# Performance work log

Hardware: AMD Instinct MI355X
Metric: run time of the kernel (lower is better)

Reference implementation:

```python
import jax, jax.numpy as jnp
import numpy as np

B = 512       # batch_size
IN = 256      # input_size
H = 512       # hidden_size
OUT = 64      # output_size
N_PAIRS = B - 1   # number of H0 persistence deaths (connected components merges)
TOL = 1e-6    # rtol for torch.isclose
ATOL = 1e-8   # torch default atol
EPS = 0.0     # homology_eps
TARGET_P = 1.0
HOM_P = 1.0
COMP_P = 0.01

_IU = np.triu_indices(B, 1)  # condensed pdist indexing, static


def _mlp(batch, W1, b1, W2, b2, W3, b3, Wout, bout):
    # FeedForward: input->hidden, (n_layers-1) hidden->hidden, hidden->output, ReLU
    h = jax.nn.relu(batch @ W1 + b1)
    h = jax.nn.relu(h @ W2 + b2)
    h = jax.nn.relu(h @ W3 + b3)
    return h @ Wout + bout


def _pdist(y):
    # condensed euclidean pairwise distances, same ordering as torch F.pdist
    d = y[_IU[0]] - y[_IU[1]]                 # [P, OUT]
    return jnp.sqrt(jnp.sum(d * d, axis=-1))  # [P]


def setup_inputs() -> dict:
    key = jax.random.key(0)
    ks = jax.random.split(key, 8)
    batch = jax.random.normal(ks[0], (B, IN), jnp.float32)
    target = jax.random.normal(ks[1], (B, OUT), jnp.float32)
    W1 = jax.random.normal(ks[2], (IN, H), jnp.float32) / np.sqrt(IN)
    W2 = jax.random.normal(ks[3], (H, H), jnp.float32) / np.sqrt(H)
    W3 = jax.random.normal(ks[4], (H, H), jnp.float32) / np.sqrt(H)
    Wout = jax.random.normal(ks[5], (H, OUT), jnp.float32) / np.sqrt(H)
    b1 = jnp.zeros((H,), jnp.float32)
    b2 = jnp.zeros((H,), jnp.float32)
    b3 = jnp.zeros((H,), jnp.float32)
    bout = jnp.zeros((OUT,), jnp.float32)
    # persistence deaths = actual critical pdist values (from the external
    # Vietoris-Rips routine in the original); sample N_PAIRS distinct entries.
    y0 = _mlp(batch, W1, b1, W2, b2, W3, b3, Wout, bout)
    pd0 = np.asarray(_pdist(y0))
    idx = np.random.default_rng(0).choice(pd0.shape[0], N_PAIRS, replace=False)
    persistence_deaths = jnp.asarray(pd0[idx], jnp.float32)
    return {"batch": batch, "target": target,
            "W1": W1, "b1": b1, "W2": W2, "b2": b2, "W3": W3, "b3": b3,
            "Wout": Wout, "bout": bout,
            "persistence_deaths": persistence_deaths}


def reference(batch, target, W1, b1, W2, b2, W3, b3, Wout, bout, persistence_deaths):
    y = _mlp(batch, W1, b1, W2, b2, W3, b3, Wout, bout)   # [B, OUT]
    y_hom = y  # normalize_for_homology = False
    pd = _pdist(y_hom)                                     # [P]
    # vectorized indicator_death over all pairs (replaces per-pair Python loop)
    mask = jnp.any(jnp.isclose(pd[:, None], persistence_deaths[None, :],
                               rtol=TOL, atol=ATOL), axis=1)      # [P] bool
    # homology_dim=0: birth_pdist = 0; norm=1 of selected (death - 0 + eps)
    homology_loss = jnp.sum(jnp.abs(jnp.where(mask, pd + EPS, 0.0)))
    target_loss = jnp.mean((target - y) ** 2)
    compactness_loss = jnp.sum(jnp.abs(y - jnp.mean(y, axis=0, keepdims=True)))
    loss = TARGET_P * target_loss + HOM_P * homology_loss + COMP_P * compactness_loss
    return loss
```

## Files before the change

kernel.cpp:

```cpp
#include <hip/hip_runtime.h>

#define B_    512
#define IN_   256
#define H_    512
#define OUT_  64
#define NDEATH (B_ - 1)
#define NSORT  512
#define RTOL_ 1e-6
#define ATOL_ 1e-8
#define NBLK  256
#define KT    32

typedef __attribute__((ext_vector_type(4))) double d4_t;

__device__ __forceinline__ void ast(double* p, double v) {
    __hip_atomic_store(p, v, __ATOMIC_RELAXED, __HIP_MEMORY_SCOPE_AGENT);
}

__device__ __forceinline__ void gbar(unsigned* cnt, unsigned nb) {
    __syncthreads();
    if (threadIdx.x == 0) {
        __hip_atomic_fetch_add(cnt, 1u, __ATOMIC_RELAXED,
                               __HIP_MEMORY_SCOPE_AGENT);
        while (__hip_atomic_load(cnt, __ATOMIC_RELAXED,
                                 __HIP_MEMORY_SCOPE_AGENT) < nb)
            __builtin_amdgcn_s_sleep(2);
    }
    __syncthreads();
}

__device__ void sort_windows(const float* __restrict__ deaths,
                             double* sd, double* slo, double* shi, int t) {
    int i1 = t + 256;
    sd[t]  = (t  < NDEATH) ? (double)deaths[t]  : 1e300;
    sd[i1] = (i1 < NDEATH) ? (double)deaths[i1] : 1e300;
    __syncthreads();
    for (int k = 2; k <= NSORT; k <<= 1) {
        for (int j = k >> 1; j > 0; j >>= 1) {
            int l = ((t & ~(j - 1)) << 1) | (t & (j - 1));
            int p = l + j;
            bool up = ((l & k) == 0);
            double a = sd[l], b = sd[p];
            if ((a > b) == up) { sd[l] = b; sd[p] = a; }
            __syncthreads();
        }
    }
    for (int i = t; i < NSORT; i += 256) {
        double d = sd[i];
        double w = ATOL_ + RTOL_ * fabs(d);
        slo[i] = d - w;
        shi[i] = d + w;
    }
    __syncthreads();
}

template <typename TIN, bool RELU>
__device__ void gemm_dev(const TIN* __restrict__ A, const float* __restrict__ W,
                         const float* __restrict__ bias, double* __restrict__ C,
                         int N, int K, int tile, int t,
                         double (&As)[2][KT][33], double (&Ws)[2][KT][33]) {
    const int lane = t & 63;
    const int wave = t >> 6;
    const int wm   = wave & 1, wn = wave >> 1;
    const int nbx  = N >> 5;
    const int row0 = (tile / nbx) << 5;
    const int col0 = (tile % nbx) << 5;

    const int akk = t & 31;
    const int amm = t >> 5;
    const int wnn = t & 31;
    const int wkk = t >> 5;
    const int nkt = K >> 5;

    TIN   ar[2][4];
    float wr[2][4];

    auto load_to = [&](int rs, int kt) {
        const int k0 = kt << 5;
        #pragma unroll
        for (int p = 0; p < 4; ++p) {
            ar[rs][p] = A[(size_t)(row0 + amm + 8 * p) * K + k0 + akk];
            wr[rs][p] = W[(size_t)(k0 + wkk + 8 * p) * N + col0 + wnn];
        }
    };
    auto stage = [&](int rs, int buf) {
        #pragma unroll
        for (int p = 0; p < 4; ++p) {
            As[buf][akk][amm + 8 * p] = (double)ar[rs][p];
            Ws[buf][wkk + 8 * p][wnn] = (double)wr[rs][p];
        }
    };

    load_to(0, 0);
    if (nkt > 1) load_to(1, 1);
    stage(0, 0);
    __syncthreads();

    d4_t c4 = {0.0, 0.0, 0.0, 0.0};
    const int mrow = wm * 16 + (lane & 15);
    const int ncol = wn * 16 + (lane & 15);
    const int kq   = lane >> 4;

    for (int kt = 0; kt < nkt; ++kt) {
        const int cur = kt & 1;
        if (kt + 2 < nkt) load_to(cur, kt + 2);
        #pragma unroll
        for (int ks = 0; ks < KT / 4; ++ks) {
            double av = As[cur][ks * 4 + kq][mrow];
            double bv = Ws[cur][ks * 4 + kq][ncol];
            c4 = __builtin_amdgcn_mfma_f64_16x16x4f64(av, bv, c4, 0, 0, 0);
        }
        __syncthreads();
        if (kt + 1 < nkt) stage(cur ^ 1, cur ^ 1);
        __syncthreads();
    }

    #pragma unroll
    for (int r = 0; r < 4; ++r) {
        int row = row0 + wm * 16 + (lane >> 4) * 4 + r;
        int col = col0 + wn * 16 + (lane & 15);
        double v = c4[r] + (double)bias[col];
        if (RELU) v = v > 0.0 ? v : 0.0;
        ast(&C[(size_t)row * N + col], v);
    }
}

__device__ void mc_dev(const float* __restrict__ target,
                       const double* __restrict__ y,
                       double* __restrict__ t_part, double* __restrict__ c_part,
                       int c, int t) {
    const int wave = t >> 6, lane = t & 63;
    double v0 = y[(size_t)t * OUT_ + c];
    double v1 = y[(size_t)(t + 256) * OUT_ + c];
    double s = v0 + v1;
    for (int off = 32; off; off >>= 1) s += __shfl_down(s, off);
    __shared__ double swm[4];
    __shared__ double smean;
    if (lane == 0) swm[wave] = s;
    __syncthreads();
    if (t == 0) smean = (swm[0] + swm[1] + swm[2] + swm[3]) / (double)B_;
    __syncthreads();
    double m = smean;
    double d0 = (double)target[(size_t)t * OUT_ + c] - v0;
    double d1 = (double)target[(size_t)(t + 256) * OUT_ + c] - v1;
    double t_s = d0 * d0 + d1 * d1;
    double c_s = fabs(v0 - m) + fabs(v1 - m);
    for (int off = 32; off; off >>= 1) {
        t_s += __shfl_down(t_s, off);
        c_s += __shfl_down(c_s, off);
    }
    __shared__ double st[4], sc[4];
    if (lane == 0) { st[wave] = t_s; sc[wave] = c_s; }
    __syncthreads();
    if (t == 0) {
        ast(&t_part[c], st[0] + st[1] + st[2] + st[3]);
        ast(&c_part[c], sc[0] + sc[1] + sc[2] + sc[3]);
    }
}

__device__ __forceinline__ double pair_val(const double* __restrict__ yrow_s,
                                           const double* __restrict__ yj,
                                           const double* __restrict__ slo,
                                           const double* __restrict__ shi) {
    double s = 0.0;
    #pragma unroll
    for (int d = 0; d < OUT_; d += 2) {
        double2 v = *(const double2*)(yj + d);
        double d0 = yrow_s[d]     - v.x;
        double d1 = yrow_s[d + 1] - v.y;
        s = fma(d0, d0, s);
        s = fma(d1, d1, s);
    }
    double pd = sqrt(s);
    int pos = 0;
    #pragma unroll
    for (int step = NSORT / 2; step; step >>= 1) {
        if (slo[pos + step - 1] <= pd) pos += step;
    }
    bool m = (pos > 0) && (shi[pos - 1] >= pd);
    return m ? pd : 0.0;
}

__device__ void pdist_dev(const double* __restrict__ y,
                          double* __restrict__ hom_part, int bid, int t,
                          double* yA, double* yB,
                          const double* slo, const double* shi) {
    const int iA = bid;
    const int iB = 510 - bid;
    if (t < OUT_)            yA[t]        = y[(size_t)iA * OUT_ + t];
    else if (t < 2 * OUT_)   yB[t - OUT_] = y[(size_t)iB * OUT_ + (t - OUT_)];
    __syncthreads();

    double local = 0.0;
    for (int j = iA + 1 + t; j < B_; j += 256)
        local += pair_val(yA, y + (size_t)j * OUT_, slo, shi);
    if (iB != iA)
        for (int j = iB + 1 + t; j < B_; j += 256)
            local += pair_val(yB, y + (size_t)j * OUT_, slo, shi);

    for (int off = 32; off; off >>= 1) local += __shfl_down(local, off);
    __shared__ double sw[4];
    int wave = t >> 6, lane = t & 63;
    if (lane == 0) sw[wave] = local;
    __syncthreads();
    if (t == 0) ast(&hom_part[bid], sw[0] + sw[1] + sw[2] + sw[3]);
}

__global__ __launch_bounds__(256) void fused_k(
    const float* __restrict__ batch, const float* __restrict__ target,
    const float* __restrict__ W1, const float* __restrict__ b1,
    const float* __restrict__ W2, const float* __restrict__ b2,
    const float* __restrict__ W3, const float* __restrict__ b3,
    const float* __restrict__ Wout, const float* __restrict__ bout,
    const float* __restrict__ deaths, float* __restrict__ out,
    double* __restrict__ hA, double* __restrict__ hB,
    double* __restrict__ hC, double* __restrict__ yv,
    double* __restrict__ hom_part, double* __restrict__ t_part,
    double* __restrict__ c_part, unsigned* __restrict__ cnt) {
    const int bid = blockIdx.x;
    const int t   = threadIdx.x;
    const int g   = bid >> 4;
    const int c   = bid & 15;
    unsigned* gc  = cnt + g * 32;

    __shared__ double As[2][KT][33];
    __shared__ double Ws[2][KT][33];
    __shared__ double slo[NSORT], shi[NSORT];
    __shared__ double yA[OUT_], yB[OUT_];
    __shared__ int    lastf;
    double* sd = &As[0][0][0];

    gemm_dev<float,  true>(batch, W1, b1, hA, H_, IN_, bid, t, As, Ws);
    gbar(&gc[0], 16);
    gemm_dev<double, true>(hA, W2, b2, hB, H_, H_, bid, t, As, Ws);
    gbar(&gc[1], 16);
    gemm_dev<double, true>(hB, W3, b3, hC, H_, H_, bid, t, As, Ws);
    gbar(&gc[2], 16);

    if (c < 2) gemm_dev<double, false>(hC, Wout, bout, yv, OUT_, H_, g * 2 + c, t, As, Ws);
    else       sort_windows(deaths, sd, slo, shi, t);

    gbar(&cnt[512], NBLK);
    if (c < 2) sort_windows(deaths, sd, slo, shi, t);

    pdist_dev(yv, hom_part, bid, t, yA, yB, slo, shi);
    if (bid < OUT_) mc_dev(target, yv, t_part, c_part, bid, t);

    __syncthreads();
    if (t == 0) {
        unsigned prev = __hip_atomic_fetch_add(&cnt[544], 1u, __ATOMIC_RELAXED,
                                               __HIP_MEMORY_SCOPE_AGENT);
        lastf = (prev == NBLK - 1);
    }
    __syncthreads();
    if (lastf) {
        double h  = __hip_atomic_load(&hom_part[t], __ATOMIC_RELAXED,
                                      __HIP_MEMORY_SCOPE_AGENT);
        double tp = 0.0, cp = 0.0;
        if (t < OUT_) {
            tp = __hip_atomic_load(&t_part[t], __ATOMIC_RELAXED,
                                   __HIP_MEMORY_SCOPE_AGENT);
            cp = __hip_atomic_load(&c_part[t], __ATOMIC_RELAXED,
                                   __HIP_MEMORY_SCOPE_AGENT);
        }
        for (int off = 32; off; off >>= 1) {
            h  += __shfl_down(h,  off);
            tp += __shfl_down(tp, off);
            cp += __shfl_down(cp, off);
        }
        __shared__ double sh[4], stp[4], scp[4];
        int wave = t >> 6, lane = t & 63;
        if (lane == 0) { sh[wave] = h; stp[wave] = tp; scp[wave] = cp; }
        __syncthreads();
        if (t == 0) {
            double hs = sh[0]  + sh[1]  + sh[2]  + sh[3];
            double ts = stp[0] + stp[1] + stp[2] + stp[3];
            double cs = scp[0] + scp[1] + scp[2] + scp[3];
            out[0] = (float)(ts / (double)(B_ * OUT_) + hs + 0.01 * cs);
        }
    }
}

extern "C" void kernel_launch(void* const* d_in, const int* in_sizes, int n_in,
                              void* d_out, int out_size, void* d_ws, size_t ws_size,
                              hipStream_t stream) {
    const float* batch  = (const float*)d_in[0];
    const float* target = (const float*)d_in[1];
    const float* W1     = (const float*)d_in[2];
    const float* b1     = (const float*)d_in[3];
    const float* W2     = (const float*)d_in[4];
    const float* b2     = (const float*)d_in[5];
    const float* W3     = (const float*)d_in[6];
    const float* b3     = (const float*)d_in[7];
    const float* Wout   = (const float*)d_in[8];
    const float* bout   = (const float*)d_in[9];
    const float* deaths = (const float*)d_in[10];
    float* out = (float*)d_out;

    double* hA       = (double*)d_ws;
    double* hB       = hA + (size_t)B_ * H_;
    double* hC       = hB + (size_t)B_ * H_;
    double* yv       = hC + (size_t)B_ * H_;
    double* hom_part = yv + (size_t)B_ * OUT_;
    double* t_part   = hom_part + NBLK;
    double* c_part   = t_part + OUT_;
    unsigned* cnt    = (unsigned*)(c_part + OUT_);

    hipMemsetAsync(cnt, 0, 576 * sizeof(unsigned), stream);

    fused_k<<<dim3(NBLK), dim3(256), 0, stream>>>(
        batch, target, W1, b1, W2, b2, W3, b3, Wout, bout, deaths, out,
        hA, hB, hC, yv, hom_part, t_part, c_part, cnt);
}
```

Before: 131.7 us.

## Add bucket LUT for death-window search and deepen GEMM register prefetch

The 9-step binary search over the sorted death windows in pair_val is replaced by a 2048-bucket lookup table built in shared memory, followed by a short linear scan. The GEMM's register prefetch goes from two to three stages so global loads are issued three k-tiles ahead. Each block now builds its own LUT, which costs extra work and shared memory. The deeper prefetch also raises register pressure.

```diff
diff --git a/kernel.cpp b/kernel.cpp
--- a/kernel.cpp
+++ b/kernel.cpp
@@ -10,6 +10,7 @@
 #define ATOL_ 1e-8
 #define NBLK  256
 #define KT    32
+#define LUTN  2048
 
 typedef __attribute__((ext_vector_type(4))) double d4_t;
 
@@ -72,8 +73,8 @@
     const int wkk = t >> 5;
     const int nkt = K >> 5;
 
-    TIN   ar[2][4];
-    float wr[2][4];
+    TIN   ar[3][4];
+    float wr[3][4];
 
     auto load_to = [&](int rs, int kt) {
         const int k0 = kt << 5;
@@ -92,8 +93,9 @@
     };
 
     load_to(0, 0);
+    stage(0, 0);
     if (nkt > 1) load_to(1, 1);
-    stage(0, 0);
+    if (nkt > 2) load_to(2, 2);
     __syncthreads();
 
     d4_t c4 = {0.0, 0.0, 0.0, 0.0};
@@ -103,7 +105,7 @@
 
     for (int kt = 0; kt < nkt; ++kt) {
         const int cur = kt & 1;
-        if (kt + 2 < nkt) load_to(cur, kt + 2);
+        if (kt + 3 < nkt) load_to(kt % 3, kt + 3);
         #pragma unroll
         for (int ks = 0; ks < KT / 4; ++ks) {
             double av = As[cur][ks * 4 + kq][mrow];
@@ -111,7 +113,7 @@
             c4 = __builtin_amdgcn_mfma_f64_16x16x4f64(av, bv, c4, 0, 0, 0);
         }
         __syncthreads();
-        if (kt + 1 < nkt) stage(cur ^ 1, cur ^ 1);
+        if (kt + 1 < nkt) stage((kt + 1) % 3, cur ^ 1);
         __syncthreads();
     }
 
@@ -161,7 +163,9 @@
 __device__ __forceinline__ double pair_val(const double* __restrict__ yrow_s,
                                            const double* __restrict__ yj,
                                            const double* __restrict__ slo,
-                                           const double* __restrict__ shi) {
+                                           const double* __restrict__ shi,
+                                           const unsigned short* __restrict__ lut,
+                                           double base, double scale) {
     double s = 0.0;
     #pragma unroll
     for (int d = 0; d < OUT_; d += 2) {
@@ -172,11 +176,11 @@
         s = fma(d1, d1, s);
     }
     double pd = sqrt(s);
-    int pos = 0;
-    #pragma unroll
-    for (int step = NSORT / 2; step; step >>= 1) {
-        if (slo[pos + step - 1] <= pd) pos += step;
-    }
+    double x = (pd - base) * scale;
+    int b = (int)x;
+    b = b < 0 ? 0 : (b > LUTN - 1 ? LUTN - 1 : b);
+    int pos = lut[b];
+    while (pos < NSORT && slo[pos] <= pd) ++pos;
     bool m = (pos > 0) && (shi[pos - 1] >= pd);
     return m ? pd : 0.0;
 }
@@ -184,19 +188,35 @@
 __device__ void pdist_dev(const double* __restrict__ y,
                           double* __restrict__ hom_part, int bid, int t,
                           double* yA, double* yB,
-                          const double* slo, const double* shi) {
+                          const double* slo, const double* shi,
+                          unsigned short* lut) {
     const int iA = bid;
     const int iB = 510 - bid;
     if (t < OUT_)            yA[t]        = y[(size_t)iA * OUT_ + t];
     else if (t < 2 * OUT_)   yB[t - OUT_] = y[(size_t)iB * OUT_ + (t - OUT_)];
+
+    const double base = slo[0];
+    double span = shi[NDEATH - 1] - base;
+    if (span < 1e-300) span = 1e-300;
+    const double scale = (double)LUTN / span;
+    const double inv   = span / (double)LUTN;
+    for (int b = t; b < LUTN; b += 256) {
+        double e = base + ((double)b - 0.001) * inv;
+        int pos = 0;
+        #pragma unroll
+        for (int step = NSORT / 2; step; step >>= 1) {
+            if (slo[pos + step - 1] <= e) pos += step;
+        }
+        lut[b] = (unsigned short)pos;
+    }
     __syncthreads();
 
     double local = 0.0;
     for (int j = iA + 1 + t; j < B_; j += 256)
-        local += pair_val(yA, y + (size_t)j * OUT_, slo, shi);
+        local += pair_val(yA, y + (size_t)j * OUT_, slo, shi, lut, base, scale);
     if (iB != iA)
         for (int j = iB + 1 + t; j < B_; j += 256)
-            local += pair_val(yB, y + (size_t)j * OUT_, slo, shi);
+            local += pair_val(yB, y + (size_t)j * OUT_, slo, shi, lut, base, scale);
 
     for (int off = 32; off; off >>= 1) local += __shfl_down(local, off);
     __shared__ double sw[4];
@@ -227,6 +247,7 @@
     __shared__ double Ws[2][KT][33];
     __shared__ double slo[NSORT], shi[NSORT];
     __shared__ double yA[OUT_], yB[OUT_];
+    __shared__ unsigned short lut[LUTN];
     __shared__ int    lastf;
     double* sd = &As[0][0][0];
 
@@ -243,7 +264,7 @@
     gbar(&cnt[512], NBLK);
     if (c < 2) sort_windows(deaths, sd, slo, shi, t);
 
-    pdist_dev(yv, hom_part, bid, t, yA, yB, slo, shi);
+    pdist_dev(yv, hom_part, bid, t, yA, yB, slo, shi, lut);
     if (bid < OUT_) mc_dev(target, yv, t_part, c_part, bid, t);
 
     __syncthreads();
```

After: 136.3 us. 1.04x slower.
